# Kernel optimization log

Hardware: AMD Instinct MI355X
Metric: run time of the kernel (lower is better)

The kernel has to match this reference:

```python
import math
import jax, jax.numpy as jnp
import numpy as np

B, T, D = 8, 2048, 512
EPS = 1e-5


def _gate(x, W, b, a, g, beta):
    # Linear -> PReLU (single shared slope a) -> LayerNorm -> sigmoid
    h = x @ W.T + b
    h = jnp.where(h >= 0, h, a * h)
    mu = jnp.mean(h, axis=-1, keepdims=True)
    var = jnp.var(h, axis=-1, keepdims=True)
    h = (h - mu) / jnp.sqrt(var + EPS) * g + beta
    return jax.nn.sigmoid(h)


def setup_inputs() -> dict:
    key = jax.random.key(0)
    ks = jax.random.split(key, 12)
    lin = lambda k: jax.random.normal(k, (D, D), jnp.float32) * 0.02
    z = jnp.zeros((D,), jnp.float32)
    o = jnp.ones((D,), jnp.float32)
    a0 = jnp.float32(0.25)  # PReLU default init
    inp = {
        "query": jax.random.normal(ks[0], (B, T, D), jnp.float32),
        "value": jax.random.normal(ks[1], (B, T, D), jnp.float32),
        "aux_emb": jax.random.normal(ks[2], (B, 1, D), jnp.float32),
        # ragged valid lengths in [T//2, T] to keep every sample realistic
        "input_len": jax.random.randint(ks[3], (B,), T // 2, T + 1),
        "Wq": lin(ks[4]), "bq": z,
        "Wqg": lin(ks[5]), "bqg": z, "aq": a0, "gq": o, "betaq": z,
        "Wkg": lin(ks[6]), "bkg": z, "ak": a0, "gk": o, "betak": z,
        "Wvg": lin(ks[7]), "bvg": z, "av": a0, "gv": o, "betav": z,
        "Wsig": lin(ks[8]), "bsig": z,
        "Wtan": lin(ks[9]), "btan": z,
    }
    return inp


def reference(query, value, aux_emb, input_len,
              Wq, bq,
              Wqg, bqg, aq, gq, betaq,
              Wkg, bkg, ak, gk, betak,
              Wvg, bvg, av, gv, betav,
              Wsig, bsig, Wtan, btan):
    q = query @ Wq.T + bq
    q = q * _gate(aux_emb, Wqg, bqg, aq, gq, betaq)          # [B,T,D]
    k = value * _gate(aux_emb, Wkg, bkg, ak, gk, betak)      # [B,T,D]
    vg = _gate(aux_emb, Wvg, bvg, av, gv, betav)             # [B,1,D]
    vg = jax.nn.sigmoid(vg @ Wsig.T + bsig) * jnp.tanh(vg @ Wtan.T + btan)
    v = value * vg                                           # [B,T,D]

    w = jnp.einsum('btd,bsd->bts', q, k) / math.sqrt(D)      # [B,T,T]
    r = jnp.arange(T)
    causal = (r[:, None] >= r[None, :]).astype(w.dtype)      # tril ones
    w = w * causal
    w = jnp.where(w == 0.0, -jnp.inf, w)  # torch quirk: exact zeros -> -inf
    L = input_len[:, None, None]                              # [B,1,1]
    invalid = (r[None, :, None] < L) & (r[None, None, :] >= L)
    w = jnp.where(invalid, -jnp.inf, w)
    p = jax.nn.softmax(w, axis=-1)
    # rows beyond input_len are padding: zero them (torch code produced NaN
    # there via -inf*0; intended semantics is zeroed padding rows)
    row_valid = (r[None, :, None] < L).astype(p.dtype)        # [B,T,1]
    p = p * row_valid
    return p @ v                                              # [B,T,D]
```

## Files before the change

### kernel.cpp

```cpp
#include <hip/hip_runtime.h>
#include <hip/hip_bf16.h>
#include <stdint.h>

#define BB 8
#define TT 2048
#define DD 512

typedef __attribute__((ext_vector_type(8))) __bf16 bf16x8;
typedef __attribute__((ext_vector_type(4))) float f32x4;

__device__ __forceinline__ unsigned short f2bf(float f) {
    unsigned u = __builtin_bit_cast(unsigned, f);
    unsigned r = u + 0x7fffu + ((u >> 16) & 1u);
    return (unsigned short)(r >> 16);
}

__device__ __forceinline__ void gload_lds16(const unsigned short* g, unsigned short* l) {
    __builtin_amdgcn_global_load_lds(
        (const __attribute__((address_space(1))) void*)g,
        (__attribute__((address_space(3))) void*)l, 16, 0, 0);
}

__global__ __launch_bounds__(256) void gates_mv1(
    const float* __restrict__ aux,
    const float* __restrict__ Wqg, const float* __restrict__ bqg, const float* __restrict__ aq,
    const float* __restrict__ Wkg, const float* __restrict__ bkg, const float* __restrict__ ak,
    const float* __restrict__ Wvg, const float* __restrict__ bvg, const float* __restrict__ av,
    float* __restrict__ h) {
    __shared__ float saux[BB * DD];
    int tid = threadIdx.x;
#pragma unroll
    for (int i = 0; i < 4; i++) {
        int idx = tid + i * 256;
        ((float4*)saux)[idx] = ((const float4*)aux)[idx];
    }
    __syncthreads();
    int wave = (blockIdx.x * 256 + tid) >> 6;
    int lane = tid & 63;
    int g = wave >> 9, r = wave & 511;
    const float* W    = (g == 0) ? Wqg : (g == 1) ? Wkg : Wvg;
    const float* bias = (g == 0) ? bqg : (g == 1) ? bkg : bvg;
    const float* alpha = (g == 0) ? aq : (g == 1) ? ak : av;
    const float4* Wrow = (const float4*)(W + (size_t)r * DD);
    float acc[BB];
#pragma unroll
    for (int b = 0; b < BB; b++) acc[b] = 0.f;
#pragma unroll
    for (int c = 0; c < 2; c++) {
        float4 w4 = Wrow[lane + c * 64];
#pragma unroll
        for (int b = 0; b < BB; b++) {
            float4 a4 = ((const float4*)(saux + b * DD))[lane + c * 64];
            acc[b] += w4.x * a4.x + w4.y * a4.y + w4.z * a4.z + w4.w * a4.w;
        }
    }
#pragma unroll
    for (int b = 0; b < BB; b++) {
#pragma unroll
        for (int s = 1; s < 64; s <<= 1) acc[b] += __shfl_xor(acc[b], s, 64);
    }
    if (lane == 0) {
        float bi = bias[r], a = alpha[0];
#pragma unroll
        for (int b = 0; b < BB; b++) {
            float v = acc[b] + bi;
            v = (v >= 0.f) ? v : a * v;
            h[(g * BB + b) * DD + r] = v;
        }
    }
}

__global__ __launch_bounds__(512) void gates_norm(
    const float* __restrict__ h,
    const float* __restrict__ gq, const float* __restrict__ betaq,
    const float* __restrict__ gk, const float* __restrict__ betak,
    const float* __restrict__ gv, const float* __restrict__ betav,
    float* __restrict__ qgate, float* __restrict__ kgate, float* __restrict__ vg) {
    int g = blockIdx.x >> 3, b = blockIdx.x & 7, tid = threadIdx.x;
    __shared__ float red[DD], red2[DD];
    float hv = h[(g * BB + b) * DD + tid];
    red[tid] = hv; red2[tid] = hv * hv;
    __syncthreads();
    for (int s = 256; s > 0; s >>= 1) {
        if (tid < s) { red[tid] += red[tid + s]; red2[tid] += red2[tid + s]; }
        __syncthreads();
    }
    float mu = red[0] * (1.f / DD);
    float var = red2[0] * (1.f / DD) - mu * mu;
    const float* gg = (g == 0) ? gq : (g == 1) ? gk : gv;
    const float* be = (g == 0) ? betaq : (g == 1) ? betak : betav;
    float val = (hv - mu) * rsqrtf(var + 1e-5f) * gg[tid] + be[tid];
    float sg = 1.f / (1.f + expf(-val));
    float* outp = (g == 0) ? qgate : (g == 1) ? kgate : vg;
    outp[b * DD + tid] = sg;
}

__global__ __launch_bounds__(256) void gates_mv2(
    const float* __restrict__ vg,
    const float* __restrict__ Wsig, const float* __restrict__ bsig,
    const float* __restrict__ Wtan, const float* __restrict__ btan,
    float* __restrict__ vgate) {
    __shared__ float svg[BB * DD];
    int tid = threadIdx.x;
#pragma unroll
    for (int i = 0; i < 4; i++) {
        int idx = tid + i * 256;
        ((float4*)svg)[idx] = ((const float4*)vg)[idx];
    }
    __syncthreads();
    int r = (blockIdx.x * 256 + tid) >> 6;
    int lane = tid & 63;
    const float4* Ws = (const float4*)(Wsig + (size_t)r * DD);
    const float4* Wt = (const float4*)(Wtan + (size_t)r * DD);
    float as_[BB], at_[BB];
#pragma unroll
    for (int b = 0; b < BB; b++) { as_[b] = 0.f; at_[b] = 0.f; }
#pragma unroll
    for (int c = 0; c < 2; c++) {
        float4 w1 = Ws[lane + c * 64];
        float4 w2 = Wt[lane + c * 64];
#pragma unroll
        for (int b = 0; b < BB; b++) {
            float4 a4 = ((const float4*)(svg + b * DD))[lane + c * 64];
            as_[b] += w1.x * a4.x + w1.y * a4.y + w1.z * a4.z + w1.w * a4.w;
            at_[b] += w2.x * a4.x + w2.y * a4.y + w2.z * a4.z + w2.w * a4.w;
        }
    }
#pragma unroll
    for (int b = 0; b < BB; b++) {
#pragma unroll
        for (int s = 1; s < 64; s <<= 1) {
            as_[b] += __shfl_xor(as_[b], s, 64);
            at_[b] += __shfl_xor(at_[b], s, 64);
        }
    }
    if (lane == 0) {
        float b1 = bsig[r], b2 = btan[r];
#pragma unroll
        for (int b = 0; b < BB; b++) {
            float s1 = 1.f / (1.f + expf(-(as_[b] + b1)));
            float s2 = tanhf(at_[b] + b2);
            vgate[b * DD + r] = s1 * s2;
        }
    }
}

__global__ __launch_bounds__(256) void convert_kernel(
    const float* __restrict__ query, const float* __restrict__ Wq,
    const float* __restrict__ value,
    const float* __restrict__ kgate, const float* __restrict__ vgate,
    unsigned short* __restrict__ queryb, unsigned short* __restrict__ Wqb,
    unsigned short* __restrict__ kb, unsigned short* __restrict__ vbT) {
    __shared__ float tile[32][33];
    int bi = blockIdx.x, tid = threadIdx.x;
    if (bi < 8192) {
        int idx = bi * 256 + tid;
        float4 q4 = ((const float4*)query)[idx];
        ushort4 oq;
        oq.x = f2bf(q4.x); oq.y = f2bf(q4.y); oq.z = f2bf(q4.z); oq.w = f2bf(q4.w);
        ((ushort4*)queryb)[idx] = oq;
    } else if (bi < 8448) {
        int idx = (bi - 8192) * 256 + tid;
        float4 w4 = ((const float4*)Wq)[idx];
        ushort4 o;
        o.x = f2bf(w4.x); o.y = f2bf(w4.y); o.z = f2bf(w4.z); o.w = f2bf(w4.w);
        ((ushort4*)Wqb)[idx] = o;
    } else {
        int vb = bi - 8448;
        int tIdx = vb & 63, dIdx = (vb >> 6) & 15, b = vb >> 10;
        int t0 = tIdx * 32, d0 = dIdx * 32;
        int tx = tid & 31, ty = tid >> 5;
        float kg = kgate[b * DD + d0 + tx];
#pragma unroll
        for (int i = 0; i < 4; i++) {
            int t = t0 + ty + i * 8;
            float v = value[((size_t)b * TT + t) * DD + d0 + tx];
            tile[ty + i * 8][tx] = v;
            kb[((size_t)b * TT + t) * DD + d0 + tx] = f2bf(v * kg);
        }
        __syncthreads();
#pragma unroll
        for (int i = 0; i < 4; i++) {
            int d = d0 + ty + i * 8;
            float g = vgate[b * DD + d];
            vbT[((size_t)b * DD + d) * TT + t0 + tx] = f2bf(tile[tx][ty + i * 8] * g);
        }
    }
}

#define GEMM_CORE(APTR, ALDA, BPTR, BLDA, KSTART, KEND)                                   \
    __shared__ __align__(16) unsigned short As[128 * 32];                                 \
    __shared__ __align__(16) unsigned short Bs[128 * 32];                                 \
    int tid = threadIdx.x;                                                                \
    int lane = tid & 63, wid = tid >> 6;                                                  \
    int wm = (wid >> 1) * 64, wn = (wid & 1) * 64;                                        \
    int lm = lane & 15, quad = lane >> 4;                                                 \
    f32x4 acc[4][4];                                                                      \
    _Pragma("unroll") for (int im = 0; im < 4; im++)                                      \
        _Pragma("unroll") for (int in = 0; in < 4; in++)                                  \
            acc[im][in] = (f32x4){0.f, 0.f, 0.f, 0.f};                                    \
    for (int k0 = (KSTART); k0 < (KEND); k0 += 32) {                                      \
        _Pragma("unroll") for (int i = 0; i < 2; i++) {                                   \
            int idx = tid * 8 + i * 2048;                                                 \
            int r = idx >> 5;                                                             \
            int cg = ((idx >> 3) & 3) ^ ((r >> 1) & 3);                                   \
            gload_lds16(&(APTR)[(size_t)r * (ALDA) + k0 + cg * 8], &As[idx]);             \
            gload_lds16(&(BPTR)[(size_t)r * (BLDA) + k0 + cg * 8], &Bs[idx]);             \
        }                                                                                 \
        __syncthreads();                                                                  \
        bf16x8 af[4], bf_[4];                                                             \
        _Pragma("unroll") for (int i = 0; i < 4; i++) {                                   \
            int row = wm + i * 16 + lm;                                                   \
            af[i] = *(const bf16x8*)&As[row * 32 + (quad ^ ((row >> 1) & 3)) * 8];        \
        }                                                                                 \
        _Pragma("unroll") for (int i = 0; i < 4; i++) {                                   \
            int row = wn + i * 16 + lm;                                                   \
            bf_[i] = *(const bf16x8*)&Bs[row * 32 + (quad ^ ((row >> 1) & 3)) * 8];       \
        }                                                                                 \
        _Pragma("unroll") for (int im = 0; im < 4; im++)                                  \
            _Pragma("unroll") for (int in = 0; in < 4; in++)                              \
                acc[im][in] = __builtin_amdgcn_mfma_f32_16x16x32_bf16(af[im], bf_[in],    \
                                                                     acc[im][in], 0, 0, 0);\
        __syncthreads();                                                                  \
    }

__global__ __launch_bounds__(256) void qgemm_kernel(
    const unsigned short* __restrict__ Amat, const unsigned short* __restrict__ Bmat,
    const float* __restrict__ bq, const float* __restrict__ qgate,
    unsigned short* __restrict__ qb) {
    int m0 = blockIdx.x * 128, n0 = blockIdx.y * 128;
    const unsigned short* Ap = Amat + (size_t)m0 * DD;
    const unsigned short* Bp = Bmat + (size_t)n0 * DD;
    GEMM_CORE(Ap, DD, Bp, DD, 0, DD)
    int b = m0 >> 11;
#pragma unroll
    for (int im = 0; im < 4; im++) {
        int row = m0 + wm + im * 16 + quad * 4;
#pragma unroll
        for (int in = 0; in < 4; in++) {
            int col = n0 + wn + in * 16 + lm;
            float bias = bq[col];
            float g = qgate[b * DD + col];
#pragma unroll
            for (int r = 0; r < 4; r++) {
                float v = (acc[im][in][r] + bias) * g;
                qb[(size_t)(row + r) * DD + col] = f2bf(v);
            }
        }
    }
}

__global__ __launch_bounds__(256) void scores_kernel(
    const unsigned short* __restrict__ qb, const unsigned short* __restrict__ kb,
    unsigned short* __restrict__ P, float* __restrict__ rowsum) {
    int b = blockIdx.z;
    int idx = blockIdx.x;
    int mt = (int)((sqrtf(8.f * idx + 1.f) - 1.f) * 0.5f);
    while ((mt + 1) * (mt + 2) / 2 <= idx) mt++;
    while (mt * (mt + 1) / 2 > idx) mt--;
    int nt = idx - mt * (mt + 1) / 2;
    int t0 = mt * 128, s0 = nt * 128;
    const unsigned short* Ap = qb + ((size_t)b * TT + t0) * DD;
    const unsigned short* Bp = kb + ((size_t)b * TT + s0) * DD;
    GEMM_CORE(Ap, DD, Bp, DD, 0, DD)
    const float scale = 0.044194173824159216f;
    unsigned short* Ptile = P + ((size_t)b * 136 + (size_t)mt * (mt + 1) / 2 + nt) * 16384;
#pragma unroll
    for (int im = 0; im < 4; im++) {
        int ltb = wm + im * 16 + quad * 4;
        float rs[4] = {0.f, 0.f, 0.f, 0.f};
#pragma unroll
        for (int in = 0; in < 4; in++) {
            int ls = wn + in * 16 + lm;
            int s = s0 + ls;
#pragma unroll
            for (int r = 0; r < 4; r++) {
                float p = (s <= t0 + ltb + r) ? expf(acc[im][in][r] * scale) : 0.f;
                Ptile[(size_t)(ltb + r) * 128 + ls] = f2bf(p);
                rs[r] += p;
            }
        }
#pragma unroll
        for (int r = 0; r < 4; r++) {
            float v = rs[r];
            v += __shfl_xor(v, 1, 64);
            v += __shfl_xor(v, 2, 64);
            v += __shfl_xor(v, 4, 64);
            v += __shfl_xor(v, 8, 64);
            if (lm == 0) atomicAdd(&rowsum[b * TT + t0 + ltb + r], v);
        }
    }
}

__global__ __launch_bounds__(256) void out_kernel(
    const unsigned short* __restrict__ P, const unsigned short* __restrict__ vbT,
    const float* __restrict__ rowsum, const int* __restrict__ input_len,
    float* __restrict__ out) {
    int nt = blockIdx.x;
    int mt2 = 31 - (int)blockIdx.y;
    int b = blockIdx.z;
    int t0 = mt2 * 64, n0 = nt * 128;
    int mt = mt2 >> 1;
    int rowoff = (mt2 & 1) * 64;
    size_t triBase = ((size_t)b * 136 + (size_t)mt * (mt + 1) / 2) * 16384;
    int kend = (mt + 1) * 128;

    __shared__ __align__(16) unsigned short As[64 * 32];
    __shared__ __align__(16) unsigned short Bs[128 * 32];
    int tid = threadIdx.x;
    int lane = tid & 63, wid = tid >> 6;
    int wm = (wid >> 1) * 32, wn = (wid & 1) * 64;
    int lm = lane & 15, quad = lane >> 4;
    f32x4 acc[2][4];
#pragma unroll
    for (int im = 0; im < 2; im++)
#pragma unroll
        for (int in = 0; in < 4; in++) acc[im][in] = (f32x4){0.f, 0.f, 0.f, 0.f};

    for (int k0 = 0; k0 < kend; k0 += 32) {
        {
            int idx = tid * 8;
            int r = idx >> 5;
            int cg = ((idx >> 3) & 3) ^ ((r >> 1) & 3);
            const unsigned short* ag = P + triBase + (size_t)(k0 >> 7) * 16384 +
                                       (size_t)(rowoff + r) * 128 + (k0 & 127) + cg * 8;
            gload_lds16(ag, &As[idx]);
        }
#pragma unroll
        for (int i = 0; i < 2; i++) {
            int idx = tid * 8 + i * 2048;
            int r = idx >> 5;
            int cg = ((idx >> 3) & 3) ^ ((r >> 1) & 3);
            gload_lds16(&vbT[(size_t)(b * DD + n0 + r) * TT + k0 + cg * 8], &Bs[idx]);
        }
        __syncthreads();
        bf16x8 af[2], bf_[4];
#pragma unroll
        for (int i = 0; i < 2; i++) {
            int row = wm + i * 16 + lm;
            af[i] = *(const bf16x8*)&As[row * 32 + (quad ^ ((row >> 1) & 3)) * 8];
        }
#pragma unroll
        for (int i = 0; i < 4; i++) {
            int row = wn + i * 16 + lm;
            bf_[i] = *(const bf16x8*)&Bs[row * 32 + (quad ^ ((row >> 1) & 3)) * 8];
        }
#pragma unroll
        for (int im = 0; im < 2; im++)
#pragma unroll
            for (int in = 0; in < 4; in++)
                acc[im][in] = __builtin_amdgcn_mfma_f32_16x16x32_bf16(af[im], bf_[in],
                                                                     acc[im][in], 0, 0, 0);
        __syncthreads();
    }

    int L = input_len[b];
#pragma unroll
    for (int im = 0; im < 2; im++) {
        int tbase = t0 + wm + im * 16 + quad * 4;
#pragma unroll
        for (int r = 0; r < 4; r++) {
            int t = tbase + r;
            float inv = 1.f / rowsum[b * TT + t];
            bool valid = (t < L);
#pragma unroll
            for (int in = 0; in < 4; in++) {
                int n = n0 + wn + in * 16 + lm;
                float o = valid ? acc[im][in][r] * inv : 0.f;
                out[((size_t)b * TT + t) * DD + n] = o;
            }
        }
    }
}

extern "C" void kernel_launch(void* const* d_in, const int* in_sizes, int n_in,
                              void* d_out, int out_size, void* d_ws, size_t ws_size,
                              hipStream_t stream) {
    const float* query = (const float*)d_in[0];
    const float* value = (const float*)d_in[1];
    const float* aux   = (const float*)d_in[2];
    const int*   ilen  = (const int*)d_in[3];
    const float* Wq    = (const float*)d_in[4];
    const float* bq    = (const float*)d_in[5];
    const float* Wqg   = (const float*)d_in[6];
    const float* bqg   = (const float*)d_in[7];
    const float* aq    = (const float*)d_in[8];
    const float* gq    = (const float*)d_in[9];
    const float* betaq = (const float*)d_in[10];
    const float* Wkg   = (const float*)d_in[11];
    const float* bkg   = (const float*)d_in[12];
    const float* ak    = (const float*)d_in[13];
    const float* gk    = (const float*)d_in[14];
    const float* betak = (const float*)d_in[15];
    const float* Wvg   = (const float*)d_in[16];
    const float* bvg   = (const float*)d_in[17];
    const float* av    = (const float*)d_in[18];
    const float* gv    = (const float*)d_in[19];
    const float* betav = (const float*)d_in[20];
    const float* Wsig  = (const float*)d_in[21];
    const float* bsig  = (const float*)d_in[22];
    const float* Wtan  = (const float*)d_in[23];
    const float* btan  = (const float*)d_in[24];

    char* ws = (char*)d_ws;
    float* qgate          = (float*)(ws + 0);
    float* kgate          = (float*)(ws + 16384);
    float* vgate          = (float*)(ws + 32768);
    float* rowsum         = (float*)(ws + 49152);
    unsigned short* Wqb   = (unsigned short*)(ws + 114688);
    unsigned short* queryb= (unsigned short*)(ws + 638976);
    unsigned short* qb    = (unsigned short*)(ws + 17416192);
    unsigned short* kb    = (unsigned short*)(ws + 34193408);
    unsigned short* vbT   = (unsigned short*)(ws + 50970624);
    unsigned short* P     = (unsigned short*)(ws + 67747840);
    float* hbuf           = (float*)(ws + 67747840);
    float* vg             = (float*)(ws + 67747840 + 49152);

    hipMemsetAsync(rowsum, 0, BB * TT * sizeof(float), stream);

    gates_mv1<<<384, 256, 0, stream>>>(aux, Wqg, bqg, aq, Wkg, bkg, ak, Wvg, bvg, av, hbuf);
    gates_norm<<<24, 512, 0, stream>>>(hbuf, gq, betaq, gk, betak, gv, betav,
                                       qgate, kgate, vg);
    gates_mv2<<<128, 256, 0, stream>>>(vg, Wsig, bsig, Wtan, btan, vgate);

    convert_kernel<<<16640, 256, 0, stream>>>(query, Wq, value, kgate, vgate,
                                              queryb, Wqb, kb, vbT);
    qgemm_kernel<<<dim3((BB * TT) / 128, DD / 128), 256, 0, stream>>>(queryb, Wqb, bq, qgate, qb);
    scores_kernel<<<dim3(136, 1, BB), 256, 0, stream>>>(qb, kb, P, rowsum);
    out_kernel<<<dim3(4, 32, BB), 256, 0, stream>>>(P, vbT, rowsum, ilen, (float*)d_out);
}
```

Measured before the change: 297.4 us.

## Fuse causal scores and PV into one attention kernel without materializing P

Replaces the separate scores and output kernels with one fused kernel. Each block owns 32 query rows and the full 512-wide output. It computes QK^T per 128-key tile, exponentiates into an LDS P tile and immediately multiplies by V. Row sums are reduced in shared memory instead of by global atomics, which removes the P round-trip through global memory, the rowsum memset and one launch. In exchange each 32-row block reloads K and V tiles, so K/V reuse per tile drops sharply, and the inner loops are small and synchronization-heavy with no double buffering.

```diff
diff --git a/kernel.cpp b/kernel.cpp
--- a/kernel.cpp
+++ b/kernel.cpp
@@ -250,127 +250,146 @@
     }
 }
 
-__global__ __launch_bounds__(256) void scores_kernel(
+__global__ __launch_bounds__(256, 2) void attn_fused(
     const unsigned short* __restrict__ qb, const unsigned short* __restrict__ kb,
-    unsigned short* __restrict__ P, float* __restrict__ rowsum) {
-    int b = blockIdx.z;
-    int idx = blockIdx.x;
-    int mt = (int)((sqrtf(8.f * idx + 1.f) - 1.f) * 0.5f);
-    while ((mt + 1) * (mt + 2) / 2 <= idx) mt++;
-    while (mt * (mt + 1) / 2 > idx) mt--;
-    int nt = idx - mt * (mt + 1) / 2;
-    int t0 = mt * 128, s0 = nt * 128;
-    const unsigned short* Ap = qb + ((size_t)b * TT + t0) * DD;
-    const unsigned short* Bp = kb + ((size_t)b * TT + s0) * DD;
-    GEMM_CORE(Ap, DD, Bp, DD, 0, DD)
+    const unsigned short* __restrict__ vbT, const int* __restrict__ input_len,
+    float* __restrict__ out) {
+    int b = blockIdx.y;
+    int mt4 = (b & 1) ? (int)blockIdx.x : 63 - (int)blockIdx.x;
+    int t0 = mt4 * 32;
+    int nst = (mt4 >> 2) + 1;
+
+    __shared__ __align__(16) unsigned short As[32 * 32];
+    __shared__ __align__(16) unsigned short Bs[128 * 32];
+    __shared__ __align__(16) unsigned short Vs[512 * 32];
+    __shared__ __align__(16) unsigned short Ps[32 * 136];
+    __shared__ float redw[4][32];
+
+    int tid = threadIdx.x, lane = tid & 63, wid = tid >> 6;
+    int lm = lane & 15, quad = lane >> 4;
+
+    const unsigned short* qB = qb + ((size_t)b * TT + t0) * DD;
+    const unsigned short* kB = kb + (size_t)b * TT * DD;
+    const unsigned short* vB = vbT + (size_t)b * DD * TT;
+
+    f32x4 oacc[2][8];
+#pragma unroll
+    for (int im = 0; im < 2; im++)
+#pragma unroll
+        for (int in = 0; in < 8; in++) oacc[im][in] = (f32x4){0.f, 0.f, 0.f, 0.f};
+    float rs[2][4] = {{0.f, 0.f, 0.f, 0.f}, {0.f, 0.f, 0.f, 0.f}};
+
     const float scale = 0.044194173824159216f;
-    unsigned short* Ptile = P + ((size_t)b * 136 + (size_t)mt * (mt + 1) / 2 + nt) * 16384;
-#pragma unroll
-    for (int im = 0; im < 4; im++) {
-        int ltb = wm + im * 16 + quad * 4;
-        float rs[4] = {0.f, 0.f, 0.f, 0.f};
-#pragma unroll
-        for (int in = 0; in < 4; in++) {
-            int ls = wn + in * 16 + lm;
-            int s = s0 + ls;
-#pragma unroll
-            for (int r = 0; r < 4; r++) {
-                float p = (s <= t0 + ltb + r) ? expf(acc[im][in][r] * scale) : 0.f;
-                Ptile[(size_t)(ltb + r) * 128 + ls] = f2bf(p);
-                rs[r] += p;
-            }
-        }
+
+    for (int st = 0; st < nst; st++) {
+        int s0 = st * 128;
+        f32x4 sacc[2][2];
+#pragma unroll
+        for (int im = 0; im < 2; im++)
+#pragma unroll
+            for (int in = 0; in < 2; in++) sacc[im][in] = (f32x4){0.f, 0.f, 0.f, 0.f};
+        for (int k0 = 0; k0 < DD; k0 += 32) {
+            if (wid < 2) {
+                int row = wid * 16 + (lane >> 2);
+                int cg = (lane & 3) ^ ((row >> 1) & 3);
+                gload_lds16(&qB[(size_t)row * DD + k0 + cg * 8], &As[wid * 512 + lane * 8]);
+            }
+#pragma unroll
+            for (int c = 0; c < 2; c++) {
+                int rb = wid * 32 + c * 16;
+                int row = rb + (lane >> 2);
+                int cg = (lane & 3) ^ ((row >> 1) & 3);
+                gload_lds16(&kB[(size_t)(s0 + row) * DD + k0 + cg * 8], &Bs[rb * 32 + lane * 8]);
+            }
+            __syncthreads();
+            bf16x8 af[2], bfr[2];
+#pragma unroll
+            for (int i = 0; i < 2; i++) {
+                int row = i * 16 + lm;
+                af[i] = *(const bf16x8*)&As[row * 32 + (quad ^ ((row >> 1) & 3)) * 8];
+            }
+#pragma unroll
+            for (int i = 0; i < 2; i++) {
+                int row = wid * 32 + i * 16 + lm;
+                bfr[i] = *(const bf16x8*)&Bs[row * 32 + (quad ^ ((row >> 1) & 3)) * 8];
+            }
+#pragma unroll
+            for (int im = 0; im < 2; im++)
+#pragma unroll
+                for (int in = 0; in < 2; in++)
+                    sacc[im][in] = __builtin_amdgcn_mfma_f32_16x16x32_bf16(af[im], bfr[in],
+                                                                          sacc[im][in], 0, 0, 0);
+            __syncthreads();
+        }
+#pragma unroll
+        for (int im = 0; im < 2; im++)
+#pragma unroll
+            for (int in = 0; in < 2; in++)
+#pragma unroll
+                for (int r = 0; r < 4; r++) {
+                    int row = im * 16 + quad * 4 + r;
+                    int col = wid * 32 + in * 16 + lm;
+                    float p = (s0 + col <= t0 + row) ? expf(sacc[im][in][r] * scale) : 0.f;
+                    Ps[row * 136 + col] = f2bf(p);
+                    rs[im][r] += p;
+                }
+        __syncthreads();
+        for (int ks = 0; ks < 128; ks += 32) {
+#pragma unroll
+            for (int c = 0; c < 8; c++) {
+                int rb = wid * 128 + c * 16;
+                int row = rb + (lane >> 2);
+                int cg = (lane & 3) ^ ((row >> 1) & 3);
+                gload_lds16(&vB[(size_t)row * TT + s0 + ks + cg * 8], &Vs[rb * 32 + lane * 8]);
+            }
+            __syncthreads();
+            bf16x8 pa[2], vf[8];
+#pragma unroll
+            for (int i = 0; i < 2; i++) {
+                int mrow = i * 16 + lm;
+                pa[i] = *(const bf16x8*)&Ps[mrow * 136 + ks + quad * 8];
+            }
+#pragma unroll
+            for (int i = 0; i < 8; i++) {
+                int row = wid * 128 + i * 16 + lm;
+                vf[i] = *(const bf16x8*)&Vs[row * 32 + (quad ^ ((row >> 1) & 3)) * 8];
+            }
+#pragma unroll
+            for (int im = 0; im < 2; im++)
+#pragma unroll
+                for (int in = 0; in < 8; in++)
+                    oacc[im][in] = __builtin_amdgcn_mfma_f32_16x16x32_bf16(pa[im], vf[in],
+                                                                          oacc[im][in], 0, 0, 0);
+            __syncthreads();
+        }
+    }
+#pragma unroll
+    for (int im = 0; im < 2; im++)
 #pragma unroll
         for (int r = 0; r < 4; r++) {
-            float v = rs[r];
+            float v = rs[im][r];
             v += __shfl_xor(v, 1, 64);
             v += __shfl_xor(v, 2, 64);
             v += __shfl_xor(v, 4, 64);
             v += __shfl_xor(v, 8, 64);
-            if (lm == 0) atomicAdd(&rowsum[b * TT + t0 + ltb + r], v);
-        }
-    }
-}
-
-__global__ __launch_bounds__(256) void out_kernel(
-    const unsigned short* __restrict__ P, const unsigned short* __restrict__ vbT,
-    const float* __restrict__ rowsum, const int* __restrict__ input_len,
-    float* __restrict__ out) {
-    int nt = blockIdx.x;
-    int mt2 = 31 - (int)blockIdx.y;
-    int b = blockIdx.z;
-    int t0 = mt2 * 64, n0 = nt * 128;
-    int mt = mt2 >> 1;
-    int rowoff = (mt2 & 1) * 64;
-    size_t triBase = ((size_t)b * 136 + (size_t)mt * (mt + 1) / 2) * 16384;
-    int kend = (mt + 1) * 128;
-
-    __shared__ __align__(16) unsigned short As[64 * 32];
-    __shared__ __align__(16) unsigned short Bs[128 * 32];
-    int tid = threadIdx.x;
-    int lane = tid & 63, wid = tid >> 6;
-    int wm = (wid >> 1) * 32, wn = (wid & 1) * 64;
-    int lm = lane & 15, quad = lane >> 4;
-    f32x4 acc[2][4];
+            if (lm == 0) redw[wid][im * 16 + quad * 4 + r] = v;
+        }
+    __syncthreads();
+    int L = input_len[b];
 #pragma unroll
     for (int im = 0; im < 2; im++)
 #pragma unroll
-        for (int in = 0; in < 4; in++) acc[im][in] = (f32x4){0.f, 0.f, 0.f, 0.f};
-
-    for (int k0 = 0; k0 < kend; k0 += 32) {
-        {
-            int idx = tid * 8;
-            int r = idx >> 5;
-            int cg = ((idx >> 3) & 3) ^ ((r >> 1) & 3);
-            const unsigned short* ag = P + triBase + (size_t)(k0 >> 7) * 16384 +
-                                       (size_t)(rowoff + r) * 128 + (k0 & 127) + cg * 8;
-            gload_lds16(ag, &As[idx]);
-        }
-#pragma unroll
-        for (int i = 0; i < 2; i++) {
-            int idx = tid * 8 + i * 2048;
-            int r = idx >> 5;
-            int cg = ((idx >> 3) & 3) ^ ((r >> 1) & 3);
-            gload_lds16(&vbT[(size_t)(b * DD + n0 + r) * TT + k0 + cg * 8], &Bs[idx]);
-        }
-        __syncthreads();
-        bf16x8 af[2], bf_[4];
-#pragma unroll
-        for (int i = 0; i < 2; i++) {
-            int row = wm + i * 16 + lm;
-            af[i] = *(const bf16x8*)&As[row * 32 + (quad ^ ((row >> 1) & 3)) * 8];
-        }
-#pragma unroll
-        for (int i = 0; i < 4; i++) {
-            int row = wn + i * 16 + lm;
-            bf_[i] = *(const bf16x8*)&Bs[row * 32 + (quad ^ ((row >> 1) & 3)) * 8];
-        }
-#pragma unroll
-        for (int im = 0; im < 2; im++)
-#pragma unroll
-            for (int in = 0; in < 4; in++)
-                acc[im][in] = __builtin_amdgcn_mfma_f32_16x16x32_bf16(af[im], bf_[in],
-                                                                     acc[im][in], 0, 0, 0);
-        __syncthreads();
-    }
-
-    int L = input_len[b];
-#pragma unroll
-    for (int im = 0; im < 2; im++) {
-        int tbase = t0 + wm + im * 16 + quad * 4;
-#pragma unroll
         for (int r = 0; r < 4; r++) {
-            int t = tbase + r;
-            float inv = 1.f / rowsum[b * TT + t];
+            int row = im * 16 + quad * 4 + r;
+            int t = t0 + row;
+            float inv = 1.f / (redw[0][row] + redw[1][row] + redw[2][row] + redw[3][row]);
             bool valid = (t < L);
 #pragma unroll
-            for (int in = 0; in < 4; in++) {
-                int n = n0 + wn + in * 16 + lm;
-                float o = valid ? acc[im][in][r] * inv : 0.f;
-                out[((size_t)b * TT + t) * DD + n] = o;
-            }
-        }
-    }
+            for (int in = 0; in < 8; in++) {
+                int n = wid * 128 + in * 16 + lm;
+                out[((size_t)b * TT + t) * DD + n] = valid ? oacc[im][in][r] * inv : 0.f;
+            }
+        }
 }
 
 extern "C" void kernel_launch(void* const* d_in, const int* in_sizes, int n_in,
@@ -406,17 +425,13 @@
     float* qgate          = (float*)(ws + 0);
     float* kgate          = (float*)(ws + 16384);
     float* vgate          = (float*)(ws + 32768);
-    float* rowsum         = (float*)(ws + 49152);
     unsigned short* Wqb   = (unsigned short*)(ws + 114688);
     unsigned short* queryb= (unsigned short*)(ws + 638976);
     unsigned short* qb    = (unsigned short*)(ws + 17416192);
     unsigned short* kb    = (unsigned short*)(ws + 34193408);
     unsigned short* vbT   = (unsigned short*)(ws + 50970624);
-    unsigned short* P     = (unsigned short*)(ws + 67747840);
     float* hbuf           = (float*)(ws + 67747840);
     float* vg             = (float*)(ws + 67747840 + 49152);
-
-    hipMemsetAsync(rowsum, 0, BB * TT * sizeof(float), stream);
 
     gates_mv1<<<384, 256, 0, stream>>>(aux, Wqg, bqg, aq, Wkg, bkg, ak, Wvg, bvg, av, hbuf);
     gates_norm<<<24, 512, 0, stream>>>(hbuf, gq, betaq, gk, betak, gv, betav,
@@ -426,6 +441,5 @@
     convert_kernel<<<16640, 256, 0, stream>>>(query, Wq, value, kgate, vgate,
                                               queryb, Wqb, kb, vbT);
     qgemm_kernel<<<dim3((BB * TT) / 128, DD / 128), 256, 0, stream>>>(queryb, Wqb, bq, qgate, qb);
-    scores_kernel<<<dim3(136, 1, BB), 256, 0, stream>>>(qb, kb, P, rowsum);
-    out_kernel<<<dim3(4, 32, BB), 256, 0, stream>>>(P, vbT, rowsum, ilen, (float*)d_out);
-}
+    attn_fused<<<dim3(64, BB), 256, 0, stream>>>(qb, kb, vbT, ilen, (float*)d_out);
+}
```

Measured after the change: 369.9 us. 1.24x slower.
